# Kernel tuning notes

Measured on AMD Instinct MI355X. Metric: run time of the kernel, lower is better.

Reference implementation:

```python
import jax, jax.numpy as jnp
import numpy as np

D_STATE = 16
D_CONV = 4


def _diag_perm(H, W):
    perm = []
    for off in range(-(H - 1), W):
        for i in range(H):
            j = i + off
            if 0 <= j < W:
                perm.append(i * W + j)
    perm = np.asarray(perm, dtype=np.int32)
    inv = np.argsort(perm).astype(np.int32)
    return perm, inv


def _mamba_block(x, W_in, conv_w, W_xproj, W_dt, b_dt, A_log, W_outm):
    # x: [B, L, E]; shared-weight SimplifiedMambaBlock, expand=1 -> d_inner = E
    Bsz, L, E = x.shape
    d_inner = W_in.shape[1] // 2
    d_state = W_xproj.shape[1] // 2
    xz = x @ W_in                              # [B, L, 2*d_inner]
    xi, z = xz[..., :d_inner], xz[..., d_inner:]
    # causal depthwise conv1d (padding=d_conv-1, trimmed to L)
    xc = jax.lax.conv_general_dilated(
        xi.transpose(0, 2, 1), conv_w, window_strides=(1,),
        padding=[(conv_w.shape[-1] - 1, 0)], feature_group_count=d_inner,
        dimension_numbers=('NCH', 'OIH', 'NCH'))
    xc = jax.nn.silu(xc.transpose(0, 2, 1))    # [B, L, d_inner]
    dtbc = xc @ W_xproj                        # [B, L, 2*d_state]
    dt = jax.nn.softplus(dtbc[..., :d_state] @ W_dt + b_dt)  # [B, L, d_inner]
    Bc = dtbc[..., d_state:]                   # [B, L, d_state]
    A = -jnp.exp(A_log)                        # [d_inner, d_state]

    def step(h, inp):
        dt_t, B_t, x_t = inp                   # [B,d_inner], [B,d_state], [B,d_inner]
        h = h * jnp.exp(A[None] * dt_t[:, :, None]) + B_t[:, None, :] * x_t[:, :, None]
        return h, h.sum(-1)

    h0 = jnp.zeros((Bsz, d_inner, d_state), x.dtype)
    _, y = jax.lax.scan(step, h0, (dt.transpose(1, 0, 2), Bc.transpose(1, 0, 2), xc.transpose(1, 0, 2)))
    y = y.transpose(1, 0, 2)                   # [B, L, d_inner]
    return (y * jax.nn.silu(z)) @ W_outm


def setup_inputs() -> dict:
    key = jax.random.key(0)
    ks = jax.random.split(key, 16)
    B, H, W, E = 8, 32, 32, 1024
    d_inner, d_state = E, D_STATE
    s = lambda n: 1.0 / np.sqrt(n)
    A = np.tile(np.arange(1, d_state + 1, dtype=np.float32), (d_inner, 1))
    return {
        'vision_features': jax.random.normal(ks[0], (B, H * W, E), jnp.float32),
        'W_input': jax.random.normal(ks[1], (E, E), jnp.float32) * s(E),
        'W_in': jax.random.normal(ks[2], (E, 2 * d_inner), jnp.float32) * s(E),
        'conv_w': jax.random.normal(ks[3], (d_inner, 1, D_CONV), jnp.float32) * s(D_CONV),
        'W_xproj': jax.random.normal(ks[4], (d_inner, 2 * d_state), jnp.float32) * s(d_inner),
        'W_dt': jax.random.normal(ks[5], (d_state, d_inner), jnp.float32) * s(d_state),
        'b_dt': jax.random.normal(ks[6], (d_inner,), jnp.float32) * 0.01,
        'A_log': jnp.asarray(np.log(A)),
        'W_outm': jax.random.normal(ks[7], (d_inner, E), jnp.float32) * s(d_inner),
        'dir_w': jnp.full((4,), 0.25, jnp.float32),
        'ln_g': jnp.ones((E,), jnp.float32),
        'ln_b': jnp.zeros((E,), jnp.float32),
        'W_outproj': jax.random.normal(ks[8], (E, E), jnp.float32) * s(E),
        'Wg1': jax.random.normal(ks[9], (E, E // 4), jnp.float32) * s(E),
        'Wg2': jax.random.normal(ks[10], (E // 4, 1), jnp.float32) * s(E // 4),
        'height': H,
        'width': W,
    }


def reference(vision_features, W_input, W_in, conv_w, W_xproj, W_dt, b_dt, A_log,
              W_outm, dir_w, ln_g, ln_b, W_outproj, Wg1, Wg2, height, width):
    B, N, E = vision_features.shape
    H, Wd = int(height), int(width)
    mamba = lambda t: _mamba_block(t, W_in, conv_w, W_xproj, W_dt, b_dt, A_log, W_outm)
    x = vision_features @ W_input              # [B, N, E]
    x2d = x.reshape(B, H, Wd, E)
    # direction 1: row-major
    out1 = mamba(x)
    # direction 2: flipped both spatial dims
    xf = jnp.flip(x2d, (1, 2)).reshape(B, N, E)
    out2 = jnp.flip(mamba(xf).reshape(B, H, Wd, E), (1, 2)).reshape(B, N, E)
    # direction 3: column-major (transpose)
    xt = x2d.transpose(0, 2, 1, 3).reshape(B, N, E)
    out3 = mamba(xt).reshape(B, Wd, H, E).transpose(0, 2, 1, 3).reshape(B, N, E)
    # direction 4: anti-diagonal scan
    perm, inv = _diag_perm(H, Wd)
    out4 = mamba(x[:, perm])[:, inv]
    fused = dir_w[0] * out1 + dir_w[1] * out2 + dir_w[2] * out3 + dir_w[3] * out4
    mu = fused.mean(-1, keepdims=True)
    var = ((fused - mu) ** 2).mean(-1, keepdims=True)
    fused = (fused - mu) * jax.lax.rsqrt(var + 1e-5) * ln_g + ln_b
    enhanced = fused @ W_outproj
    g = jax.nn.sigmoid(jax.nn.silu(vision_features.mean(1, keepdims=True) @ Wg1) @ Wg2)  # [B,1,1]
    return vision_features + g * enhanced
```

## Files before the change

kernel.cpp:

```cpp
#include <hip/hip_runtime.h>

typedef unsigned short u16;
typedef unsigned int u32;
typedef short v8s __attribute__((ext_vector_type(8)));
typedef float v4f __attribute__((ext_vector_type(4)));
typedef float v2f __attribute__((ext_vector_type(2)));

#define B_SZ 8
#define HH 32
#define WW 32
#define NN 1024
#define M1 (B_SZ * NN)
#define M4 (4 * M1)
#define NCHUNK 16
#define CLEN 64
#define CTB 8

__device__ __forceinline__ float bf2f(u16 u) {
    u32 x = ((u32)u) << 16;
    return __builtin_bit_cast(float, x);
}
__device__ __forceinline__ u16 f2bf(float f) {
    u32 x = __builtin_bit_cast(u32, f);
    x = x + 0x7fffu + ((x >> 16) & 1u);
    return (u16)(x >> 16);
}
__device__ __forceinline__ float rcp_(float x) { return __builtin_amdgcn_rcpf(x); }
__device__ __forceinline__ float sigmoidf_(float x) { return rcp_(1.f + __expf(-x)); }
__device__ __forceinline__ float ldf(const void* p, size_t i, int fin) {
    return fin ? ((const float*)p)[i] : bf2f(((const u16*)p)[i]);
}
__device__ __forceinline__ u16 ldbf(const void* p, size_t i, int fin) {
    return fin ? f2bf(((const float*)p)[i]) : ((const u16*)p)[i];
}
__device__ __forceinline__ void gload_lds16(const u16* g, u16* l) {
    __builtin_amdgcn_global_load_lds(
        (const __attribute__((address_space(1))) unsigned int*)g,
        (__attribute__((address_space(3))) unsigned int*)l, 16, 0, 0);
}
__device__ __forceinline__ int dirmap(int d, int t, const int* __restrict__ perm3) {
    if (d == 0) return t;
    if (d == 1) return (NN - 1) - t;
    if (d == 2) return (t & (HH - 1)) * WW + (t >> 5);
    return perm3[t];
}

__global__ void detect_dtype(const u16* __restrict__ raw, int* __restrict__ flags) {
    if (threadIdx.x == 0 && blockIdx.x == 0) {
        int ok = 0;
        for (int i = 0; i < 512; i++) {
            int e = (raw[i] >> 7) & 0xFF;
            ok += (e >= 100 && e <= 140) ? 1 : 0;
        }
        flags[0] = (ok < 460) ? 1 : 0;
    }
}

__global__ __launch_bounds__(256) void convert_bf(const void* __restrict__ src,
                                                  u16* __restrict__ dst,
                                                  const int* __restrict__ flags, int n) {
    int fin = flags[0];
    int i = blockIdx.x * 256 + threadIdx.x;
    if (i < n) dst[i] = ldbf(src, (size_t)i, fin);
}

__global__ __launch_bounds__(256) void zero_f32(float* __restrict__ p, int n) {
    int i = blockIdx.x * 256 + threadIdx.x;
    if (i < n) p[i] = 0.f;
}

__global__ void diag_perm_init(int* __restrict__ perm, int* __restrict__ inv) {
    int t = blockIdx.x * blockDim.x + threadIdx.x;
    if (t >= NN) return;
    int i = t / WW, j = t % WW;
    int off = j - i;
    int start = 0;
    for (int o = -(HH - 1); o < off; ++o) {
        int lo = (0 > -o) ? 0 : -o;
        int hi = (HH - 1 < WW - 1 - o) ? (HH - 1) : (WW - 1 - o);
        start += (hi - lo + 1);
    }
    int lo0 = (0 > -off) ? 0 : -off;
    int r = start + (i - lo0);
    perm[r] = t;
    inv[t] = r;
}

__global__ __launch_bounds__(256) void transpose_pad(const void* __restrict__ src,
                                                     u16* __restrict__ dst,
                                                     int K, int Nsrc,
                                                     const int* __restrict__ flags) {
    int fin = flags[0];
    __shared__ u16 tile[32][33];
    int k0 = blockIdx.x * 32, n0 = blockIdx.y * 32;
    int tx = threadIdx.x & 31, ty = threadIdx.x >> 5;
#pragma unroll
    for (int i = 0; i < 4; i++) {
        int k = k0 + ty + i * 8, n = n0 + tx;
        tile[ty + i * 8][tx] = (n < Nsrc) ? ldbf(src, (size_t)k * Nsrc + n, fin) : (u16)0;
    }
    __syncthreads();
#pragma unroll
    for (int i = 0; i < 4; i++) {
        int n = n0 + ty + i * 8, k = k0 + tx;
        dst[(size_t)n * K + k] = tile[tx][ty + i * 8];
    }
}

template <int EM>
__global__ __launch_bounds__(256, 4) void gemm128(const u16* __restrict__ A,
                                                  const u16* __restrict__ Bt,
                                                  void* __restrict__ out0,
                                                  void* __restrict__ out1,
                                                  int M, int N, int K,
                                                  const int* __restrict__ flags,
                                                  const void* __restrict__ aux0,
                                                  const float* __restrict__ aux1) {
    int fin = flags[0];
    __shared__ __align__(16) u16 As[128][32];
    __shared__ __align__(16) u16 Bs[128][32];
    int tid = threadIdx.x;
    int wave = tid >> 6, lane = tid & 63, quad = lane >> 4, l16 = lane & 15;
    int wm = wave >> 1, wn = wave & 1;
    int m0 = blockIdx.x * 128, n0 = blockIdx.y * 128;
    int r = tid >> 2, p = tid & 3;
    int sA = ((p ^ ((r >> 1) & 3))) * 8;

    const u16* rA0 = A + (size_t)(m0 + r) * K;
    const u16* rA1 = A + (size_t)(m0 + 64 + r) * K;
    const u16* rB0 = Bt + (size_t)(n0 + r) * K;
    const u16* rB1 = Bt + (size_t)(n0 + 64 + r) * K;

    v4f acc[4][4];
#pragma unroll
    for (int i = 0; i < 4; i++)
#pragma unroll
        for (int j = 0; j < 4; j++) acc[i][j] = (v4f){0.f, 0.f, 0.f, 0.f};

    int swf = ((l16 >> 1) & 3);
    for (int k0 = 0; k0 < K; k0 += 32) {
        gload_lds16(rA0 + k0 + sA, &As[r][p * 8]);
        gload_lds16(rA1 + k0 + sA, &As[64 + r][p * 8]);
        gload_lds16(rB0 + k0 + sA, &Bs[r][p * 8]);
        gload_lds16(rB1 + k0 + sA, &Bs[64 + r][p * 8]);
        __syncthreads();
        v8s af[4], bf[4];
#pragma unroll
        for (int i = 0; i < 4; i++)
            af[i] = *(const v8s*)&As[wm * 64 + i * 16 + l16][(quad ^ swf) * 8];
#pragma unroll
        for (int j = 0; j < 4; j++)
            bf[j] = *(const v8s*)&Bs[wn * 64 + j * 16 + l16][(quad ^ swf) * 8];
#pragma unroll
        for (int i = 0; i < 4; i++)
#pragma unroll
            for (int j = 0; j < 4; j++)
                acc[i][j] = __builtin_amdgcn_mfma_f32_16x16x32_bf16(af[i], bf[j],
                                                                    acc[i][j], 0, 0, 0);
        __syncthreads();
    }

#pragma unroll
    for (int i = 0; i < 4; i++) {
#pragma unroll
        for (int j = 0; j < 4; j++) {
#pragma unroll
            for (int rr = 0; rr < 4; rr++) {
                int row = m0 + wm * 64 + i * 16 + quad * 4 + rr;
                int col = n0 + wn * 64 + j * 16 + l16;
                float v = acc[i][j][rr];
                size_t oi = (size_t)row * N + col;
                if (EM == 0) {
                    ((u16*)out0)[oi] = f2bf(v);
                } else if (EM == 1) {
                    if (col < 1024) {
                        ((u16*)out0)[(size_t)row * 1024 + col] = f2bf(v);
                    } else {
                        float sz = v * sigmoidf_(v);
                        ((u16*)out1)[(size_t)row * 1024 + (col - 1024)] = f2bf(sz);
                    }
                } else {
                    float g = aux1[row >> 10];
                    float res = ldf(aux0, oi, fin) + g * v;
                    if (fin) ((float*)out0)[oi] = res;
                    else ((u16*)out0)[oi] = f2bf(res);
                }
            }
        }
    }
}

__global__ __launch_bounds__(256) void gemm_dtbc(const u16* __restrict__ A,
                                                 const u16* __restrict__ Bt,
                                                 float* __restrict__ out0,
                                                 int M, int N, int K) {
    __shared__ u16 As[64][32];
    __shared__ u16 Bs[64][32];
    int tid = threadIdx.x;
    int wave = tid >> 6, lane = tid & 63, quad = lane >> 4, l16 = lane & 15;
    int m0 = blockIdx.x * 64;
    int lr = tid >> 2, p = tid & 3;
    int sA = ((p ^ ((lr >> 1) & 3))) * 8;
    const u16* arow = A + (size_t)(m0 + lr) * K;
    const u16* brow = Bt + (size_t)lr * K;
    v4f acc[4];
#pragma unroll
    for (int j = 0; j < 4; j++) acc[j] = (v4f){0.f, 0.f, 0.f, 0.f};
    int swf = ((l16 >> 1) & 3);
    for (int k0 = 0; k0 < K; k0 += 32) {
        uint4 av = *(const uint4*)(arow + k0 + sA);
        uint4 bv = *(const uint4*)(brow + k0 + sA);
        *(uint4*)&As[lr][p * 8] = av;
        *(uint4*)&Bs[lr][p * 8] = bv;
        __syncthreads();
        v8s af = *(const v8s*)&As[wave * 16 + l16][(quad ^ swf) * 8];
#pragma unroll
        for (int j = 0; j < 4; j++) {
            v8s bf = *(const v8s*)&Bs[j * 16 + l16][(quad ^ swf) * 8];
            acc[j] = __builtin_amdgcn_mfma_f32_16x16x32_bf16(af, bf, acc[j], 0, 0, 0);
        }
        __syncthreads();
    }
#pragma unroll
    for (int j = 0; j < 4; j++)
#pragma unroll
        for (int rr = 0; rr < 4; rr++) {
            int row = m0 + wave * 16 + quad * 4 + rr;
            int col = j * 16 + l16;
            out0[(size_t)row * N + col] = acc[j][rr];
        }
}

__global__ __launch_bounds__(256) void conv_tile(const u16* __restrict__ xi,
                                                 const void* __restrict__ cw,
                                                 u16* __restrict__ xc4,
                                                 const int* __restrict__ flags,
                                                 const int* __restrict__ perm3) {
    int fin = flags[0];
    int gblk = blockIdx.x;
    int d = gblk >> 10, blk = gblk & 1023;
    int b = blk >> 7, tc = blk & 127;
    int t0 = tc * CTB;
    __shared__ u16 rows[CTB + 3][1024];
    __shared__ int sp[CTB + 3];
    if (threadIdx.x < CTB + 3) {
        int tt = t0 - 3 + (int)threadIdx.x;
        sp[threadIdx.x] = (tt >= 0) ? dirmap(d, tt, perm3) : -1;
    }
    __syncthreads();
    for (int i = threadIdx.x; i < (CTB + 3) * 128; i += 256) {
        int r = i >> 7, off = (i & 127) * 8;
        int src = sp[r];
        uint4 v = make_uint4(0, 0, 0, 0);
        if (src >= 0)
            v = *(const uint4*)(xi + ((size_t)(b * 1024 + src)) * 1024 + off);
        *(uint4*)&rows[r][off] = v;
    }
    int e0 = threadIdx.x * 4;
    float w[4][4];
#pragma unroll
    for (int ee = 0; ee < 4; ee++)
#pragma unroll
        for (int k = 0; k < 4; k++)
            w[ee][k] = ldf(cw, (size_t)(e0 + ee) * 4 + k, fin);
    __syncthreads();
    u16* outp = xc4 + (size_t)d * M1 * 1024;
#pragma unroll
    for (int t = 0; t < CTB; t++) {
        float a[4] = {0.f, 0.f, 0.f, 0.f};
#pragma unroll
        for (int k = 0; k < 4; k++) {
            uint2 v = *(const uint2*)&rows[t + k][e0];
            const u16* vs = (const u16*)&v;
#pragma unroll
            for (int ee = 0; ee < 4; ee++)
                a[ee] += w[ee][k] * bf2f(vs[ee]);
        }
        u16 o[4];
#pragma unroll
        for (int ee = 0; ee < 4; ee++) o[ee] = f2bf(a[ee] * sigmoidf_(a[ee]));
        *(uint2*)(outp + ((size_t)(b * 1024 + t0 + t)) * 1024 + e0) = *(const uint2*)o;
    }
}

#define SHUF_LO(q) __builtin_shufflevector(q, q, 0, 1)
#define SHUF_HI(q) __builtin_shufflevector(q, q, 2, 3)
#define SCAN_TLOOP(FASTV)                                                      \
    for (int t = 0; t < CLEN; t++) {                                           \
        float xn = 0.f, zn = 0.f;                                              \
        if (t + 1 < CLEN) {                                                    \
            xn = bf2f(xcyz[ix + 1024]);                                        \
            if (PASS == 3) zn = bf2f(zb[zbase + (size_t)s_perm[t + 1] * 1024]);\
        }                                                                      \
        v4f q0 = *(const v4f*)&sdt[t][0];                                      \
        v4f q1 = *(const v4f*)&sdt[t][4];                                      \
        v4f q2 = *(const v4f*)&sdt[t][8];                                      \
        v4f q3 = *(const v4f*)&sdt[t][12];                                     \
        v2f xpv = {bd, 0.f};                                                   \
        xpv += SHUF_LO(q0) * wdt2[0];                                          \
        xpv += SHUF_HI(q0) * wdt2[1];                                          \
        xpv += SHUF_LO(q1) * wdt2[2];                                          \
        xpv += SHUF_HI(q1) * wdt2[3];                                          \
        xpv += SHUF_LO(q2) * wdt2[4];                                          \
        xpv += SHUF_HI(q2) * wdt2[5];                                          \
        xpv += SHUF_LO(q3) * wdt2[6];                                          \
        xpv += SHUF_HI(q3) * wdt2[7];                                          \
        float xp = xpv.x + xpv.y;                                              \
        float ex = __expf(xp);                                                 \
        v4f r0 = *(const v4f*)&sdt[t][16];                                     \
        v4f r1 = *(const v4f*)&sdt[t][20];                                     \
        v4f r2 = *(const v4f*)&sdt[t][24];                                     \
        v4f r3 = *(const v4f*)&sdt[t][28];                                     \
        v2f bc[8];                                                             \
        bc[0] = SHUF_LO(r0); bc[1] = SHUF_HI(r0);                              \
        bc[2] = SHUF_LO(r1); bc[3] = SHUF_HI(r1);                              \
        bc[4] = SHUF_LO(r2); bc[5] = SHUF_HI(r2);                              \
        bc[6] = SHUF_LO(r3); bc[7] = SHUF_HI(r3);                              \
        v2f acc2 = {0.f, 0.f};                                                 \
        if (FASTV) {                                                           \
            float E = rcp_(1.f + ex);           \
            v2f Ev; Ev.x = E; Ev.y = E * E;                                    \
            v2f Estep; Estep.x = Ev.y; Estep.y = Ev.y;                         \
            _Pragma("unroll")                                                  \
            for (int p = 0; p < 8; p++) {                                      \
                h2[p] = h2[p] * Ev + bc[p] * xv;                               \
                acc2 += h2[p];                                                 \
                Ev *= Estep;                                                   \
            }                                                                  \
            if (PASS == 1) ds *= E;                   \
        } else {                                                               \
            float dtv = (xp > 15.f) ? xp : __logf(1.f + ex);                   \
            _Pragma("unroll")                                                  \
            for (int p = 0; p < 8; p++) {                                      \
                v2f es;                                                        \
                es.x = __expf(Ae2[p].x * dtv);                                 \
                es.y = __expf(Ae2[p].y * dtv);                                 \
                h2[p] = h2[p] * es + bc[p] * xv;                               \
                acc2 += h2[p];                                                 \
            }                                                                  \
            if (PASS == 1) ds += dtv;                                          \
        }                                                                      \
        if (PASS == 3) {                                                       \
            float accv = acc2.x + acc2.y;                                      \
            xcyz[ix] = f2bf(accv * zv * wd);  \
        }                                                                      \
        ix += 1024;                                                            \
        xv = xn;                                                               \
        zv = zn;                                                               \
    }

template <int PASS>
__global__ __launch_bounds__(256) void scan_chunk(const float* __restrict__ dtbc,
                                                  u16* __restrict__ xcyz,
                                                  const u16* __restrict__ zb,
                                                  const void* __restrict__ A_log,
                                                  const void* __restrict__ W_dt,
                                                  const void* __restrict__ b_dt,
                                                  const int* __restrict__ flags,
                                                  float* __restrict__ hend,
                                                  float* __restrict__ dtsum,
                                                  const void* __restrict__ dirw,
                                                  const int* __restrict__ perm3) {
    int fin = flags[0];
    int bid = blockIdx.x;
    int ec = bid & 3, c = (bid >> 2) & (NCHUNK - 1), b = (bid >> 6) & 7, d = bid >> 9;
    int e = ec * 256 + threadIdx.x;
    size_t row0 = (size_t)d * M1 + b * 1024 + c * CLEN;
    size_t cix  = (size_t)d * (8 * NCHUNK) + b * NCHUNK + c;
    __shared__ float sdt[CLEN][32];
    __shared__ int s_perm[CLEN];
    {
        const float* src = dtbc + row0 * 64;
        for (int i = threadIdx.x; i < CLEN * 8; i += 256) {
            int t = i >> 3, f = i & 7;
            *(float4*)&sdt[t][f * 4] = *(const float4*)(src + (size_t)t * 64 + f * 4);
        }
        if (PASS == 3 && threadIdx.x < CLEN)
            s_perm[threadIdx.x] = dirmap(d, c * CLEN + (int)threadIdx.x, perm3);
    }
    v2f Ae2[8], wdt2[8];
    bool fast = true;
#pragma unroll
    for (int p = 0; p < 8; p++) {
        float a0 = -__expf(ldf(A_log, (size_t)e * 16 + 2 * p, fin));
        float a1 = -__expf(ldf(A_log, (size_t)e * 16 + 2 * p + 1, fin));
        Ae2[p].x = a0;
        Ae2[p].y = a1;
        fast = fast && fabsf(a0 + (float)(2 * p + 1)) < 1e-3f * (2 * p + 1)
                    && fabsf(a1 + (float)(2 * p + 2)) < 1e-3f * (2 * p + 2);
    }
#pragma unroll
    for (int p = 0; p < 8; p++) {
        wdt2[p].x = ldf(W_dt, (size_t)(2 * p) * 1024 + e, fin);
        wdt2[p].y = ldf(W_dt, (size_t)(2 * p + 1) * 1024 + e, fin);
    }
    float bd = ldf(b_dt, e, fin);
    float wd = (PASS == 3) ? ldf(dirw, d, fin) : 0.f;
    v2f h2[8];
    if (PASS == 1) {
#pragma unroll
        for (int p = 0; p < 8; p++) h2[p] = (v2f){0.f, 0.f};
    } else {
#pragma unroll
        for (int p = 0; p < 8; p++) {
            h2[p].x = hend[(cix * 16 + 2 * p) * 1024 + e];
            h2[p].y = hend[(cix * 16 + 2 * p + 1) * 1024 + e];
        }
    }
    __syncthreads();
    float ds = fast ? 1.f : 0.f;
    size_t ix = row0 * 1024 + e;
    size_t zbase = (size_t)b * 1024 * 1024 + e;
    float xv = bf2f(xcyz[ix]);
    float zv = (PASS == 3) ? bf2f(zb[zbase + (size_t)s_perm[0] * 1024]) : 0.f;
    if (fast) {
        SCAN_TLOOP(true)
    } else {
        SCAN_TLOOP(false)
    }
    if (PASS == 1) {
#pragma unroll
        for (int p = 0; p < 8; p++) {
            hend[(cix * 16 + 2 * p) * 1024 + e] = h2[p].x;
            hend[(cix * 16 + 2 * p + 1) * 1024 + e] = h2[p].y;
        }
        dtsum[cix * 1024 + e] = ds;
    }
}

__global__ __launch_bounds__(256) void scan_combine2(float* __restrict__ hend,
                                                     const float* __restrict__ dtsum,
                                                     const void* __restrict__ A_log,
                                                     const int* __restrict__ flags) {
    int fin = flags[0];
    int bid = blockIdx.x;
    int ec = bid & 3, s = (bid >> 2) & 15, b = (bid >> 6) & 7, d = bid >> 9;
    int e = ec * 256 + threadIdx.x;
    bool fast = true;
#pragma unroll
    for (int s2 = 0; s2 < 16; s2++) {
        float a = -__expf(ldf(A_log, (size_t)e * 16 + s2, fin));
        fast = fast && fabsf(a + (float)(s2 + 1)) < 1e-3f * (s2 + 1);
    }
    float Ae = -__expf(ldf(A_log, (size_t)e * 16 + s, fin));
    float H = 0.f;
    size_t base = (size_t)d * (8 * NCHUNK) + (size_t)b * NCHUNK;
    for (int c = 0; c < NCHUNK; c++) {
        size_t cix = base + c;
        float ds = dtsum[cix * 1024 + e];
        float decay;
        if (fast) {
            float r = 1.f, bb = ds;
            int n = s + 1;
            while (n) {
                if (n & 1) r *= bb;
                bb *= bb;
                n >>= 1;
            }
            decay = r;
        } else {
            decay = __expf(Ae * ds);
        }
        size_t idx = (cix * 16 + s) * 1024 + e;
        float loc = hend[idx];
        hend[idx] = H;
        H = loc + decay * H;
    }
}

__global__ __launch_bounds__(256) void ln4_kernel(const u16* __restrict__ y4,
                                                  const void* __restrict__ ln_g,
                                                  const void* __restrict__ ln_b,
                                                  const int* __restrict__ flags,
                                                  const int* __restrict__ inv3,
                                                  u16* __restrict__ fn) {
    int fin = flags[0];
    int row = blockIdx.x;
    int b = row >> 10, q = row & 1023;
    int t1 = 1023 - q;
    int t2 = ((q & 31) << 5) | (q >> 5);
    int t3 = inv3[q];
    const u16* p0 = y4 + ((size_t)(b * 1024 + q)) * 1024;
    const u16* p1 = y4 + ((size_t)(M1 + b * 1024 + t1)) * 1024;
    const u16* p2 = y4 + ((size_t)(2 * M1 + b * 1024 + t2)) * 1024;
    const u16* p3 = y4 + ((size_t)(3 * M1 + b * 1024 + t3)) * 1024;
    int e0 = threadIdx.x * 4;
    uint2 a0 = *(const uint2*)(p0 + e0);
    uint2 a1 = *(const uint2*)(p1 + e0);
    uint2 a2 = *(const uint2*)(p2 + e0);
    uint2 a3 = *(const uint2*)(p3 + e0);
    const u16* s0 = (const u16*)&a0;
    const u16* s1 = (const u16*)&a1;
    const u16* s2 = (const u16*)&a2;
    const u16* s3 = (const u16*)&a3;
    float v[4];
    float sum = 0.f, sq = 0.f;
#pragma unroll
    for (int j = 0; j < 4; j++) {
        float f = bf2f(s0[j]) + bf2f(s1[j]) + bf2f(s2[j]) + bf2f(s3[j]);
        v[j] = f;
        sum += f;
        sq += f * f;
    }
    __shared__ float r1[256], r2[256];
    r1[threadIdx.x] = sum;
    r2[threadIdx.x] = sq;
    __syncthreads();
    for (int s = 128; s > 0; s >>= 1) {
        if (threadIdx.x < s) {
            r1[threadIdx.x] += r1[threadIdx.x + s];
            r2[threadIdx.x] += r2[threadIdx.x + s];
        }
        __syncthreads();
    }
    float mu = r1[0] * (1.f / 1024.f);
    float var = r2[0] * (1.f / 1024.f) - mu * mu;
    float rs = rsqrtf(var + 1e-5f);
    u16 o[4];
#pragma unroll
    for (int j = 0; j < 4; j++) {
        int e = e0 + j;
        o[j] = f2bf((v[j] - mu) * rs * ldf(ln_g, e, fin) + ldf(ln_b, e, fin));
    }
    *(uint2*)(fn + (size_t)row * 1024 + e0) = *(const uint2*)o;
}

__global__ __launch_bounds__(256) void gate_partial(const u16* __restrict__ vfb,
                                                    float* __restrict__ meanv) {
    int b = blockIdx.x >> 4, tc = blockIdx.x & 15;
    float s[4] = {0.f, 0.f, 0.f, 0.f};
    const u16* base = vfb + ((size_t)b * 1024 + tc * 64) * 1024;
    for (int t = 0; t < 64; t++) {
#pragma unroll
        for (int k = 0; k < 4; k++)
            s[k] += bf2f(base[(size_t)t * 1024 + threadIdx.x + k * 256]);
    }
#pragma unroll
    for (int k = 0; k < 4; k++)
        atomicAdd(&meanv[b * 1024 + threadIdx.x + k * 256], s[k]);
}

__global__ __launch_bounds__(256) void gate_mv(const float* __restrict__ meanv,
                                               const void* __restrict__ Wg1,
                                               const int* __restrict__ flags,
                                               float* __restrict__ gpart) {
    int fin = flags[0];
    int kc = blockIdx.x, j = threadIdx.x;
    __shared__ float mv[8][32];
    if (threadIdx.x < 8 * 32) {
        int b = threadIdx.x >> 5, kk = threadIdx.x & 31;
        mv[b][kk] = meanv[b * 1024 + kc * 32 + kk] * (1.f / 1024.f);
    }
    __syncthreads();
    float acc[8];
#pragma unroll
    for (int b = 0; b < 8; b++) acc[b] = 0.f;
    for (int kk = 0; kk < 32; kk++) {
        float w = ldf(Wg1, (size_t)(kc * 32 + kk) * 256 + j, fin);
#pragma unroll
        for (int b = 0; b < 8; b++) acc[b] += mv[b][kk] * w;
    }
#pragma unroll
    for (int b = 0; b < 8; b++) atomicAdd(&gpart[b * 256 + j], acc[b]);
}

__global__ __launch_bounds__(256) void gate_fin2(const float* __restrict__ gpart,
                                                 const void* __restrict__ Wg2,
                                                 const int* __restrict__ flags,
                                                 float* __restrict__ g) {
    int fin = flags[0];
    int b = blockIdx.x, j = threadIdx.x;
    __shared__ float red[256];
    float a = gpart[b * 256 + j];
    float si = a * sigmoidf_(a);
    red[j] = si * ldf(Wg2, j, fin);
    __syncthreads();
    for (int st = 128; st > 0; st >>= 1) {
        if (j < st) red[j] += red[j + st];
        __syncthreads();
    }
    if (j == 0) g[b] = sigmoidf_(red[0]);
}

extern "C" void kernel_launch(void* const* d_in, const int* in_sizes, int n_in,
                              void* d_out, int out_size, void* d_ws, size_t ws_size,
                              hipStream_t stream) {
    const void* vf_raw  = d_in[0];
    const void* W_input = d_in[1];
    const void* W_in    = d_in[2];
    const void* conv_w  = d_in[3];
    const void* W_xproj = d_in[4];
    const void* W_dt    = d_in[5];
    const void* b_dt    = d_in[6];
    const void* A_log   = d_in[7];
    const void* W_outm  = d_in[8];
    const void* dir_w   = d_in[9];
    const void* ln_g    = d_in[10];
    const void* ln_b    = d_in[11];
    const void* W_outpj = d_in[12];
    const void* Wg1     = d_in[13];
    const void* Wg2     = d_in[14];

    char* ws = (char*)d_ws;
    size_t off = 0;
    auto alloc = [&](size_t bytes) -> void* {
        void* p = ws + off;
        off = (off + bytes + 255) & ~(size_t)255;
        return p;
    };
    int*   flags = (int*)alloc(256);
    int*   perm3 = (int*)alloc(NN * 4);
    int*   inv3  = (int*)alloc(NN * 4);
    float* meanv = (float*)alloc(8 * 1024 * 4);
    float* gpart = (float*)alloc(8 * 256 * 4);
    float* gbuf  = (float*)alloc(64);
    u16*   WtI   = (u16*)alloc((size_t)1024 * 1024 * 2);
    u16*   WtIn  = (u16*)alloc((size_t)2048 * 1024 * 2);
    u16*   WtXp  = (u16*)alloc((size_t)64 * 1024 * 2);
    u16*   WtOm  = (u16*)alloc((size_t)1024 * 1024 * 2);
    u16*   WtOp  = (u16*)alloc((size_t)1024 * 1024 * 2);
    u16*   vfb   = (u16*)alloc((size_t)M1 * 1024 * 2);
    u16*   xbuf  = (u16*)alloc((size_t)M1 * 1024 * 2);
    float* tail32= (float*)alloc((size_t)M1 * 1024 * 4);
    u16*   xi    = (u16*)alloc((size_t)M1 * 1024 * 2);
    u16*   zb    = (u16*)alloc((size_t)M1 * 1024 * 2);
    u16*   xc4   = (u16*)alloc((size_t)M4 * 1024 * 2);
    float* dtbc4 = (float*)alloc((size_t)M4 * 64 * 4);
    float* dtsum4= (float*)alloc((size_t)4 * 8 * NCHUNK * 1024 * 4);
    float* hend4 = (float*)vfb;
    u16*   y4    = (u16*)vfb;
    (void)tail32;

    detect_dtype<<<1, 64, 0, stream>>>((const u16*)vf_raw, flags);
    convert_bf<<<(M1 * 1024) / 256, 256, 0, stream>>>(vf_raw, vfb, flags, M1 * 1024);
    diag_perm_init<<<4, 256, 0, stream>>>(perm3, inv3);
    transpose_pad<<<dim3(32, 32), 256, 0, stream>>>(W_input, WtI, 1024, 1024, flags);
    transpose_pad<<<dim3(32, 64), 256, 0, stream>>>(W_in, WtIn, 1024, 2048, flags);
    transpose_pad<<<dim3(32, 2), 256, 0, stream>>>(W_xproj, WtXp, 1024, 32, flags);
    transpose_pad<<<dim3(32, 32), 256, 0, stream>>>(W_outm, WtOm, 1024, 1024, flags);
    transpose_pad<<<dim3(32, 32), 256, 0, stream>>>(W_outpj, WtOp, 1024, 1024, flags);
    zero_f32<<<40, 256, 0, stream>>>(meanv, 8 * 1024 + 8 * 256);

    gate_partial<<<128, 256, 0, stream>>>(vfb, meanv);
    gate_mv<<<32, 256, 0, stream>>>(meanv, Wg1, flags, gpart);
    gate_fin2<<<8, 256, 0, stream>>>(gpart, Wg2, flags, gbuf);

    gemm128<0><<<dim3(64, 8), 256, 0, stream>>>(
        vfb, WtI, xbuf, nullptr, M1, 1024, 1024, flags, nullptr, nullptr);
    gemm128<1><<<dim3(64, 16), 256, 0, stream>>>(
        xbuf, WtIn, xi, zb, M1, 2048, 1024, flags, nullptr, nullptr);

    conv_tile<<<4096, 256, 0, stream>>>(xi, conv_w, xc4, flags, perm3);
    gemm_dtbc<<<512, 256, 0, stream>>>(xc4, WtXp, dtbc4, M4, 64, 1024);
    scan_chunk<1><<<2048, 256, 0, stream>>>(dtbc4, xc4, zb, A_log, W_dt, b_dt,
                                            flags, hend4, dtsum4, dir_w, perm3);
    scan_combine2<<<2048, 256, 0, stream>>>(hend4, dtsum4, A_log, flags);
    scan_chunk<3><<<2048, 256, 0, stream>>>(dtbc4, xc4, zb, A_log, W_dt, b_dt,
                                            flags, hend4, dtsum4, dir_w, perm3);

    gemm128<0><<<dim3(256, 8), 256, 0, stream>>>(
        xc4, WtOm, y4, nullptr, M4, 1024, 1024, flags, nullptr, nullptr);

    u16* fn = xi;
    ln4_kernel<<<M1, 256, 0, stream>>>(y4, ln_g, ln_b, flags, inv3, fn);
    gemm128<4><<<dim3(64, 8), 256, 0, stream>>>(
        fn, WtOp, d_out, nullptr, M1, 1024, 1024, flags, vf_raw, gbuf);
}
```

Measured before the change: 642.1 us.

## Fold input projection into in_proj weight via precomputed weight-product GEMM

Computes the product of W_input and W_in once per call as a small weight-only GEMM, then applies the fused weight directly to the vision features. This removes one full activation-sized GEMM and its intermediate buffer write/read. The GEMM kernel gains templated tile sizes so the small weight product uses 64x64 tiles. The fused weight is rounded to bf16, which changes numerical rounding slightly.

```diff
diff --git a/kernel.cpp b/kernel.cpp
--- a/kernel.cpp
+++ b/kernel.cpp
@@ -107,7 +107,7 @@
     }
 }
 
-template <int EM>
+template <int EM, int WI, int WJ>
 __global__ __launch_bounds__(256, 4) void gemm128(const u16* __restrict__ A,
                                                   const u16* __restrict__ Bt,
                                                   void* __restrict__ out0,
@@ -116,13 +116,15 @@
                                                   const int* __restrict__ flags,
                                                   const void* __restrict__ aux0,
                                                   const float* __restrict__ aux1) {
-    int fin = flags[0];
-    __shared__ __align__(16) u16 As[128][32];
-    __shared__ __align__(16) u16 Bs[128][32];
+    constexpr int BM = WI * 32;
+    constexpr int BN = WJ * 32;
+    int fin = flags[0];
+    __shared__ __align__(16) u16 As[BM][32];
+    __shared__ __align__(16) u16 Bs[BN][32];
     int tid = threadIdx.x;
     int wave = tid >> 6, lane = tid & 63, quad = lane >> 4, l16 = lane & 15;
     int wm = wave >> 1, wn = wave & 1;
-    int m0 = blockIdx.x * 128, n0 = blockIdx.y * 128;
+    int m0 = blockIdx.x * BM, n0 = blockIdx.y * BN;
     int r = tid >> 2, p = tid & 3;
     int sA = ((p ^ ((r >> 1) & 3))) * 8;
 
@@ -131,43 +133,45 @@
     const u16* rB0 = Bt + (size_t)(n0 + r) * K;
     const u16* rB1 = Bt + (size_t)(n0 + 64 + r) * K;
 
-    v4f acc[4][4];
-#pragma unroll
-    for (int i = 0; i < 4; i++)
-#pragma unroll
-        for (int j = 0; j < 4; j++) acc[i][j] = (v4f){0.f, 0.f, 0.f, 0.f};
+    v4f acc[WI][WJ];
+#pragma unroll
+    for (int i = 0; i < WI; i++)
+#pragma unroll
+        for (int j = 0; j < WJ; j++) acc[i][j] = (v4f){0.f, 0.f, 0.f, 0.f};
 
     int swf = ((l16 >> 1) & 3);
     for (int k0 = 0; k0 < K; k0 += 32) {
         gload_lds16(rA0 + k0 + sA, &As[r][p * 8]);
-        gload_lds16(rA1 + k0 + sA, &As[64 + r][p * 8]);
+        if constexpr (WI == 4)
+            gload_lds16(rA1 + k0 + sA, &As[64 + r][p * 8]);
         gload_lds16(rB0 + k0 + sA, &Bs[r][p * 8]);
-        gload_lds16(rB1 + k0 + sA, &Bs[64 + r][p * 8]);
+        if constexpr (WJ == 4)
+            gload_lds16(rB1 + k0 + sA, &Bs[64 + r][p * 8]);
         __syncthreads();
-        v8s af[4], bf[4];
-#pragma unroll
-        for (int i = 0; i < 4; i++)
-            af[i] = *(const v8s*)&As[wm * 64 + i * 16 + l16][(quad ^ swf) * 8];
-#pragma unroll
-        for (int j = 0; j < 4; j++)
-            bf[j] = *(const v8s*)&Bs[wn * 64 + j * 16 + l16][(quad ^ swf) * 8];
-#pragma unroll
-        for (int i = 0; i < 4; i++)
-#pragma unroll
-            for (int j = 0; j < 4; j++)
+        v8s af[WI], bf[WJ];
+#pragma unroll
+        for (int i = 0; i < WI; i++)
+            af[i] = *(const v8s*)&As[wm * (WI * 16) + i * 16 + l16][(quad ^ swf) * 8];
+#pragma unroll
+        for (int j = 0; j < WJ; j++)
+            bf[j] = *(const v8s*)&Bs[wn * (WJ * 16) + j * 16 + l16][(quad ^ swf) * 8];
+#pragma unroll
+        for (int i = 0; i < WI; i++)
+#pragma unroll
+            for (int j = 0; j < WJ; j++)
                 acc[i][j] = __builtin_amdgcn_mfma_f32_16x16x32_bf16(af[i], bf[j],
                                                                     acc[i][j], 0, 0, 0);
         __syncthreads();
     }
 
 #pragma unroll
-    for (int i = 0; i < 4; i++) {
-#pragma unroll
-        for (int j = 0; j < 4; j++) {
+    for (int i = 0; i < WI; i++) {
+#pragma unroll
+        for (int j = 0; j < WJ; j++) {
 #pragma unroll
             for (int rr = 0; rr < 4; rr++) {
-                int row = m0 + wm * 64 + i * 16 + quad * 4 + rr;
-                int col = n0 + wn * 64 + j * 16 + l16;
+                int row = m0 + wm * (WI * 16) + i * 16 + quad * 4 + rr;
+                int col = n0 + wn * (WJ * 16) + j * 16 + l16;
                 float v = acc[i][j][rr];
                 size_t oi = (size_t)row * N + col;
                 if (EM == 0) {
@@ -614,8 +618,9 @@
     float* meanv = (float*)alloc(8 * 1024 * 4);
     float* gpart = (float*)alloc(8 * 256 * 4);
     float* gbuf  = (float*)alloc(64);
-    u16*   WtI   = (u16*)alloc((size_t)1024 * 1024 * 2);
+    u16*   WiB   = (u16*)alloc((size_t)1024 * 1024 * 2);
     u16*   WtIn  = (u16*)alloc((size_t)2048 * 1024 * 2);
+    u16*   WtF   = (u16*)alloc((size_t)2048 * 1024 * 2);
     u16*   WtXp  = (u16*)alloc((size_t)64 * 1024 * 2);
     u16*   WtOm  = (u16*)alloc((size_t)1024 * 1024 * 2);
     u16*   WtOp  = (u16*)alloc((size_t)1024 * 1024 * 2);
@@ -630,25 +635,27 @@
     float* hend4 = (float*)vfb;
     u16*   y4    = (u16*)vfb;
     (void)tail32;
+    (void)xbuf;
 
     detect_dtype<<<1, 64, 0, stream>>>((const u16*)vf_raw, flags);
     convert_bf<<<(M1 * 1024) / 256, 256, 0, stream>>>(vf_raw, vfb, flags, M1 * 1024);
     diag_perm_init<<<4, 256, 0, stream>>>(perm3, inv3);
-    transpose_pad<<<dim3(32, 32), 256, 0, stream>>>(W_input, WtI, 1024, 1024, flags);
+    convert_bf<<<(1024 * 1024) / 256, 256, 0, stream>>>(W_input, WiB, flags, 1024 * 1024);
     transpose_pad<<<dim3(32, 64), 256, 0, stream>>>(W_in, WtIn, 1024, 2048, flags);
     transpose_pad<<<dim3(32, 2), 256, 0, stream>>>(W_xproj, WtXp, 1024, 32, flags);
     transpose_pad<<<dim3(32, 32), 256, 0, stream>>>(W_outm, WtOm, 1024, 1024, flags);
     transpose_pad<<<dim3(32, 32), 256, 0, stream>>>(W_outpj, WtOp, 1024, 1024, flags);
     zero_f32<<<40, 256, 0, stream>>>(meanv, 8 * 1024 + 8 * 256);
 
+    gemm128<0, 2, 2><<<dim3(32, 16), 256, 0, stream>>>(
+        WtIn, WiB, WtF, nullptr, 2048, 1024, 1024, flags, nullptr, nullptr);
+
     gate_partial<<<128, 256, 0, stream>>>(vfb, meanv);
     gate_mv<<<32, 256, 0, stream>>>(meanv, Wg1, flags, gpart);
     gate_fin2<<<8, 256, 0, stream>>>(gpart, Wg2, flags, gbuf);
 
-    gemm128<0><<<dim3(64, 8), 256, 0, stream>>>(
-        vfb, WtI, xbuf, nullptr, M1, 1024, 1024, flags, nullptr, nullptr);
-    gemm128<1><<<dim3(64, 16), 256, 0, stream>>>(
-        xbuf, WtIn, xi, zb, M1, 2048, 1024, flags, nullptr, nullptr);
+    gemm128<1, 4, 4><<<dim3(64, 16), 256, 0, stream>>>(
+        vfb, WtF, xi, zb, M1, 2048, 1024, flags, nullptr, nullptr);
 
     conv_tile<<<4096, 256, 0, stream>>>(xi, conv_w, xc4, flags, perm3);
     gemm_dtbc<<<512, 256, 0, stream>>>(xc4, WtXp, dtbc4, M4, 64, 1024);
@@ -658,11 +665,11 @@
     scan_chunk<3><<<2048, 256, 0, stream>>>(dtbc4, xc4, zb, A_log, W_dt, b_dt,
                                             flags, hend4, dtsum4, dir_w, perm3);
 
-    gemm128<0><<<dim3(256, 8), 256, 0, stream>>>(
+    gemm128<0, 4, 4><<<dim3(256, 8), 256, 0, stream>>>(
         xc4, WtOm, y4, nullptr, M4, 1024, 1024, flags, nullptr, nullptr);
 
     u16* fn = xi;
     ln4_kernel<<<M1, 256, 0, stream>>>(y4, ln_g, ln_b, flags, inv3, fn);
-    gemm128<4><<<dim3(64, 8), 256, 0, stream>>>(
+    gemm128<4, 4, 4><<<dim3(64, 8), 256, 0, stream>>>(
         fn, WtOp, d_out, nullptr, M1, 1024, 1024, flags, vf_raw, gbuf);
 }
```

New measurement: 636.2 us (median of 2 runs). About the same (-0.9%).
